# Optimization experiments

Measured on AMD Instinct MI355X. Metric: run time of the kernel, lower is better.

The kernel has to match this reference:

```python
import jax, jax.numpy as jnp
import numpy as np

S, N, C_M, C_Z, C, H = 256, 384, 64, 128, 32, 8


def _layer_norm(x, w, b, eps=1e-5):
    mu = x.mean(axis=-1, keepdims=True)
    var = x.var(axis=-1, keepdims=True)
    return (x - mu) / jnp.sqrt(var + eps) * w + b


def setup_inputs() -> dict:
    key = jax.random.key(0)
    ks = jax.random.split(key, 8)
    m = jax.random.normal(ks[0], (S, N, C_M), dtype=jnp.float32)
    z = jax.random.normal(ks[1], (N, N, C_Z), dtype=jnp.float32)
    single_mask = jax.random.bernoulli(ks[2], 0.9, (N,))
    scale = 0.02
    return {
        "m": m,
        "z": z,
        "single_mask": single_mask,
        "ln_m_w": jnp.ones((C_M,), jnp.float32),
        "ln_m_b": jnp.zeros((C_M,), jnp.float32),
        "ln_z_w": jnp.ones((C_Z,), jnp.float32),
        "ln_z_b": jnp.zeros((C_Z,), jnp.float32),
        "w_v": jax.random.normal(ks[3], (C_M, H * C), jnp.float32) * scale,
        "w_b": jax.random.normal(ks[4], (C_Z, H), jnp.float32) * scale,
        "w_g": jax.random.normal(ks[5], (C_M, H * C), jnp.float32) * scale,
        "w_out": jax.random.normal(ks[6], (H * C, C_M), jnp.float32) * scale,
    }


def reference(m, z, single_mask, ln_m_w, ln_m_b, ln_z_w, ln_z_b, w_v, w_b, w_g, w_out):
    # m: [s, i, c_m], z: [i, j, c_z], single_mask: [j] bool
    m_ln = _layer_norm(m, ln_m_w, ln_m_b)
    v = (m_ln @ w_v).reshape(S, N, H, C)          # [s, j, h, c]
    b = _layer_norm(z, ln_z_w, ln_z_b) @ w_b      # [i, j, h]
    g = jax.nn.sigmoid(m_ln @ w_g)                # [s, i, h*c]
    # mask broadcast over j axis: [..., None, :, None]
    b = b + jnp.where(single_mask[None, :, None], 0.0, -1e9)
    w = jax.nn.softmax(b, axis=-2)                # softmax over j
    o = jnp.einsum('ijh,sjhc->sihc', w, v)        # [s, i, h, c]
    o = g * o.reshape(S, N, H * C)
    return o @ w_out                               # [s, i, c_m]
```

## Files before the change

kernel.cpp:

```cpp
#include <hip/hip_runtime.h>
#include <math.h>


#define SS 256
#define NN 384
#define CM 64
#define CZ 128
#define HH 8
#define HC 256
#define NV 25165824

typedef __attribute__((ext_vector_type(8))) short short8v;
typedef __attribute__((ext_vector_type(8))) unsigned short ushort8v;
typedef __attribute__((ext_vector_type(4))) unsigned short ushort4v;
typedef __attribute__((ext_vector_type(4))) float f32x4;

static __device__ __forceinline__ float bf2f(unsigned short u) {
    union { unsigned int i; float f; } x; x.i = ((unsigned int)u) << 16; return x.f;
}
static __device__ __forceinline__ unsigned short f2bf(float f) {
    union { float f; unsigned int i; } x; x.f = f;
    unsigned int r = x.i + 0x7FFFu + ((x.i >> 16) & 1u);
    return (unsigned short)(r >> 16);
}
static __device__ __forceinline__ void gload_lds16(const void* g, void* l) {
    __builtin_amdgcn_global_load_lds((const __attribute__((address_space(1))) void*)g,
                                     (__attribute__((address_space(3))) void*)l, 16, 0, 0);
}

__global__ __launch_bounds__(384) void k0_mask(const unsigned int* __restrict__ mu,
                                               float* __restrict__ mterm)
{
    __shared__ int byteLayout;
    if (threadIdx.x == 0) byteLayout = 0;
    __syncthreads();
    if (threadIdx.x < 96) {
        unsigned int u = mu[threadIdx.x];
        if (u != 0u && u != 1u && u != 0x3F800000u) atomicOr(&byteLayout, 1);
    }
    __syncthreads();
    const int j = threadIdx.x;
    int val;
    if (byteLayout) val = ((const unsigned char*)mu)[j];
    else            val = (mu[j] != 0u);
    mterm[j] = val ? 0.0f : -1e9f;
}

__global__ __launch_bounds__(256) void k1a_stageB(
    const float* __restrict__ w_v, const float* __restrict__ w_g,
    unsigned short* __restrict__ BTg)
{
    const int col = blockIdx.x * 4 + (threadIdx.x >> 6);
    const int k   = threadIdx.x & 63;
    float w = (col < 256) ? w_v[k * 256 + col] : w_g[k * 256 + (col - 256)];
    BTg[col * 64 + (k ^ ((col & 7) << 3))] = f2bf(w);
}

__global__ __launch_bounds__(128) void k2a_stageW(
    const float* __restrict__ lnw, const float* __restrict__ lnb, const float* __restrict__ w_b,
    unsigned short* __restrict__ w2bf, float* __restrict__ consts)
{
    __shared__ float pA[128][8], pB[128][8];
    const int c = threadIdx.x;
    float lw = lnw[c], lb = lnb[c];
    float4 wb0 = *(const float4*)&w_b[c * 8];
    float4 wb1 = *(const float4*)&w_b[c * 8 + 4];
    float wv[8] = {wb0.x, wb0.y, wb0.z, wb0.w, wb1.x, wb1.y, wb1.z, wb1.w};
    #pragma unroll
    for (int h = 0; h < 8; h++) {
        w2bf[h * CZ + c]       = f2bf(lw * wv[h]);
        w2bf[(8 + h) * CZ + c] = 0;
        pA[c][h] = lw * wv[h];
        pB[c][h] = lb * wv[h];
    }
    __syncthreads();
    if (c < 8) {
        float A = 0.f, B = 0.f;
        for (int q = 0; q < 128; q++) { A += pA[q][c]; B += pB[q][c]; }
        consts[c] = A; consts[16 + c] = B;
        consts[8 + c] = 0.f; consts[24 + c] = 0.f;
    }
}

__global__ __launch_bounds__(256) void k1n_ln(
    const float* __restrict__ m, const float* __restrict__ lnw, const float* __restrict__ lnb,
    unsigned short* __restrict__ mln)
{
    const int tid = threadIdx.x, wid = tid >> 6, lane = tid & 63;
    const int rowBase = blockIdx.x * 64 + wid * 16;
    const float lw = lnw[lane], lb = lnb[lane];
    #pragma unroll 4
    for (int rr = 0; rr < 16; rr++) {
        int row = rowBase + rr;
        float x = m[(size_t)row * CM + lane];
        float s1 = x, s2 = x * x;
        #pragma unroll
        for (int off = 32; off; off >>= 1) {
            s1 += __shfl_xor(s1, off);
            s2 += __shfl_xor(s2, off);
        }
        float mu  = s1 * (1.0f / CM);
        float var = s2 * (1.0f / CM) - mu * mu;
        float y = (x - mu) * rsqrtf(var + 1e-5f) * lw + lb;
        mln[(size_t)row * CM + (lane ^ ((row & 7) << 3))] = f2bf(y);
    }
}

__global__ __launch_bounds__(256) void k1b_vg(
    const unsigned short* __restrict__ BTg, const unsigned short* __restrict__ mln,
    unsigned short* __restrict__ vT, unsigned short* __restrict__ gout)
{
    __shared__ unsigned short Wl[16384];
    __shared__ unsigned short Al[4096];
    const int tid = threadIdx.x, wid = tid >> 6, lane = tid & 63;
    const int rl = lane & 15, kc = lane >> 4;
    const int rowBase = blockIdx.x * 64;
    const int s = rowBase / NN, j0 = rowBase - s * NN;
    const int fam = blockIdx.y;

    #pragma unroll
    for (int it = 0; it < 8; it++) {
        int eoff = (wid * 8 + it) * 512;
        gload_lds16(BTg + fam * 16384 + eoff + lane * 8, (void*)((char*)Wl + eoff * 2));
    }
    #pragma unroll
    for (int it = 0; it < 2; it++) {
        int eoff = (wid * 2 + it) * 512;
        gload_lds16(mln + (size_t)rowBase * CM + eoff + lane * 8, (void*)((char*)Al + eoff * 2));
    }
    __syncthreads();

    f32x4 acc[4][4] = {};
    #pragma unroll
    for (int ks = 0; ks < 2; ks++) {
        short8v wf[4], al[4];
        #pragma unroll
        for (int q = 0; q < 4; q++) {
            int col = wid * 64 + q * 16 + rl;
            wf[q] = *(const short8v*)&Wl[(col * 64 + ks * 32 + kc * 8) ^ ((col & 7) << 3)];
            int row = q * 16 + rl;
            al[q] = *(const short8v*)&Al[(row * 64 + ks * 32 + kc * 8) ^ ((row & 7) << 3)];
        }
        if (fam == 0) {
            #pragma unroll
            for (int mi = 0; mi < 4; mi++)
                #pragma unroll
                for (int nf = 0; nf < 4; nf++)
                    acc[mi][nf] = __builtin_amdgcn_mfma_f32_16x16x32_bf16(al[mi], wf[nf], acc[mi][nf], 0, 0, 0);
        } else {
            #pragma unroll
            for (int mi = 0; mi < 4; mi++)
                #pragma unroll
                for (int nf = 0; nf < 4; nf++)
                    acc[mi][nf] = __builtin_amdgcn_mfma_f32_16x16x32_bf16(wf[mi], al[nf], acc[mi][nf], 0, 0, 0);
        }
    }

    if (fam == 0) {
        #pragma unroll
        for (int mi = 0; mi < 4; mi++) {
            const int jb = j0 + mi * 16 + kc * 4;
            #pragma unroll
            for (int nf = 0; nf < 4; nf++) {
                int hc = wid * 64 + nf * 16 + rl;
                size_t vrow = (size_t)((hc >> 5) * 8192 + s * 32 + (hc & 31));
                ushort4v o4;
                #pragma unroll
                for (int r = 0; r < 4; r++) o4[r] = f2bf(acc[mi][nf][r]);
                *(ushort4v*)&vT[vrow * NN + jb] = o4;
            }
        }
    } else {
        #pragma unroll
        for (int mi = 0; mi < 4; mi++) {
            const int hcb = wid * 64 + mi * 16 + kc * 4;
            #pragma unroll
            for (int nf = 0; nf < 4; nf++) {
                int row = rowBase + nf * 16 + rl;
                ushort4v o4;
                #pragma unroll
                for (int r = 0; r < 4; r++)
                    o4[r] = f2bf(1.0f / (1.0f + expf(-acc[mi][nf][r])));
                *(ushort4v*)&gout[(size_t)row * HC + hcb] = o4;
            }
        }
    }
}

__global__ __launch_bounds__(256) void k2_mfma(
    const float* __restrict__ z, const unsigned short* __restrict__ w2bf,
    const float* __restrict__ consts, const float* __restrict__ mterm,
    unsigned short* __restrict__ wbl)
{
    __shared__ float st[4][16][2];
    const int tid = threadIdx.x, wid = tid >> 6, lane = tid & 63;
    const int rl = lane & 15, kc = lane >> 4;
    const int rowBase = blockIdx.x * 64 + wid * 16;
    const int i = rowBase / NN, j0 = rowBase - i * NN;
    const float* zr = z + (size_t)(rowBase + rl) * CZ + kc * 8;

    float s1 = 0.f, s2 = 0.f;
    short8v af[4];
    #pragma unroll
    for (int ks = 0; ks < 4; ks++) {
        float4 z0 = *(const float4*)(zr + ks * 32);
        float4 z1 = *(const float4*)(zr + ks * 32 + 4);
        float zz[8] = {z0.x, z0.y, z0.z, z0.w, z1.x, z1.y, z1.z, z1.w};
        short8v a;
        #pragma unroll
        for (int q = 0; q < 8; q++) {
            s1 += zz[q];
            s2 += zz[q] * zz[q];
            a[q] = (short)f2bf(zz[q]);
        }
        af[ks] = a;
    }
    s1 += __shfl_xor(s1, 16); s2 += __shfl_xor(s2, 16);
    s1 += __shfl_xor(s1, 32); s2 += __shfl_xor(s2, 32);
    if (kc == 0) { st[wid][rl][0] = s1; st[wid][rl][1] = s2; }

    f32x4 acc = {};
    #pragma unroll
    for (int ks = 0; ks < 4; ks++) {
        short8v b = *(const short8v*)&w2bf[rl * CZ + ks * 32 + kc * 8];
        acc = __builtin_amdgcn_mfma_f32_16x16x32_bf16(af[ks], b, acc, 0, 0, 0);
    }
    __syncthreads();

    const float Ah = consts[rl], Bh = consts[16 + rl];
    unsigned short pv[4];
    #pragma unroll
    for (int reg = 0; reg < 4; reg++) {
        int r = 4 * kc + reg;
        float S1 = st[wid][r][0], S2 = st[wid][r][1];
        float mu   = S1 * (1.0f / CZ);
        float var  = S2 * (1.0f / CZ) - mu * mu;
        float rstd = rsqrtf(var + 1e-5f);
        float b = rstd * acc[reg] - rstd * mu * Ah + Bh + mterm[j0 + r];
        pv[reg] = f2bf(b);
    }
    if (rl < 8) {
        ushort4v o4 = {pv[0], pv[1], pv[2], pv[3]};
        *(ushort4v*)&wbl[((size_t)rl * NN + i) * NN + j0 + 4 * kc] = o4;
    }
}

__global__ __launch_bounds__(256) void k3_softmax(unsigned short* __restrict__ wbl)
{
    const int tid = threadIdx.x, wave = tid >> 6, lane = tid & 63;
    const int row = blockIdx.x * 4 + wave;
    unsigned short* p = wbl + (size_t)row * NN;
    float x[6];
    float mx = -1e30f;
    #pragma unroll
    for (int e = 0; e < 6; e++) { x[e] = bf2f(p[lane + e * 64]); mx = fmaxf(mx, x[e]); }
    #pragma unroll
    for (int off = 32; off; off >>= 1) mx = fmaxf(mx, __shfl_xor(mx, off));
    float sum = 0.f;
    #pragma unroll
    for (int e = 0; e < 6; e++) { x[e] = expf(x[e] - mx); sum += x[e]; }
    #pragma unroll
    for (int off = 32; off; off >>= 1) sum += __shfl_xor(sum, off);
    float inv = 1.0f / sum;
    #pragma unroll
    for (int e = 0; e < 6; e++) p[lane + e * 64] = f2bf(x[e] * inv);
}

__global__ __launch_bounds__(256) void k4_mfma(
    const unsigned short* __restrict__ wbf, const unsigned short* __restrict__ vT,
    unsigned short* __restrict__ ob)
{
    __shared__ unsigned short Al[128 * 32];
    __shared__ unsigned short Bl[128 * 32];
    const int tid  = threadIdx.x;
    const int wid  = tid >> 6, lane = tid & 63;
    const int wm   = wid >> 1, wn = wid & 1;
    const int h    = blockIdx.z;
    const int i0   = blockIdx.y * 128;
    const int n0   = blockIdx.x * 128;
    const unsigned short* Ag = wbf + (size_t)h * NN * NN;
    const unsigned short* Bg = vT  + (size_t)h * 8192 * NN;

    f32x4 acc[4][4] = {};

    const int lrow = lane >> 2, lchunk = lane & 3;
    for (int k0 = 0; k0 < NN; k0 += 32) {
        #pragma unroll
        for (int q = 0; q < 2; q++) {
            int issue = wid * 2 + q;
            int r = issue * 16 + lrow;
            gload_lds16(Ag + (size_t)(i0 + r) * NN + k0 + lchunk * 8,
                        (void*)((char*)Al + issue * 1024));
            gload_lds16(Bg + (size_t)(n0 + r) * NN + k0 + lchunk * 8,
                        (void*)((char*)Bl + issue * 1024));
        }
        __syncthreads();

        short8v a[4], b[4];
        #pragma unroll
        for (int mi = 0; mi < 4; mi++)
            a[mi] = *(const short8v*)&Al[(wm * 64 + mi * 16 + (lane & 15)) * 32 + (lane >> 4) * 8];
        #pragma unroll
        for (int ni = 0; ni < 4; ni++)
            b[ni] = *(const short8v*)&Bl[(wn * 64 + ni * 16 + (lane & 15)) * 32 + (lane >> 4) * 8];
        #pragma unroll
        for (int mi = 0; mi < 4; mi++)
            #pragma unroll
            for (int ni = 0; ni < 4; ni++)
                acc[mi][ni] = __builtin_amdgcn_mfma_f32_16x16x32_bf16(a[mi], b[ni], acc[mi][ni], 0, 0, 0);
        __syncthreads();
    }

    #pragma unroll
    for (int mi = 0; mi < 4; mi++) {
        const int ibase = i0 + wm * 64 + mi * 16 + ((lane >> 4) << 2);
        #pragma unroll
        for (int ni = 0; ni < 4; ni++) {
            const int n = n0 + wn * 64 + ni * 16 + (lane & 15);
            const int s = n >> 5, c = n & 31;
            #pragma unroll
            for (int r = 0; r < 4; r++)
                ob[((size_t)s * NN + (ibase + r)) * HC + (h << 5) + c] = f2bf(acc[mi][ni][r]);
        }
    }
}

__global__ __launch_bounds__(256) void k5_mfma(
    const unsigned short* __restrict__ ob, const unsigned short* __restrict__ g,
    const float* __restrict__ w_out, float* __restrict__ out)
{
    __shared__ unsigned short WT[64 * 256];
    const int tid = threadIdx.x, wid = tid >> 6, lane = tid & 63;
    #pragma unroll
    for (int e = 0; e < 16; e++) {
        int fidx = (tid + e * 256) * 4;
        float4 w4 = *(const float4*)&w_out[fidx];
        int k = fidx >> 6, c0 = fidx & 63;
        float wv[4] = {w4.x, w4.y, w4.z, w4.w};
        #pragma unroll
        for (int q = 0; q < 4; q++) {
            int c = c0 + q;
            WT[(((c << 8) + k)) ^ ((c & 7) << 3)] = f2bf(wv[q]);
        }
    }
    __syncthreads();

    const size_t rowbase = (size_t)blockIdx.x * 64 + wid * 16;
    const int arow = lane & 15, achunk = lane >> 4;
    const unsigned short* op = ob + (rowbase + arow) * HC + achunk * 8;
    const unsigned short* gp = g  + (rowbase + arow) * HC + achunk * 8;

    f32x4 acc[4] = {};
    #pragma unroll
    for (int ks = 0; ks < 8; ks++) {
        ushort8v o8 = *(const ushort8v*)(op + ks * 32);
        ushort8v g8 = *(const ushort8v*)(gp + ks * 32);
        short8v a;
        #pragma unroll
        for (int q = 0; q < 8; q++)
            a[q] = (short)f2bf(bf2f(o8[q]) * bf2f(g8[q]));
        #pragma unroll
        for (int nf = 0; nf < 4; nf++) {
            const int c = nf * 16 + arow;
            short8v b = *(const short8v*)&WT[(((c << 8) + ks * 32 + achunk * 8)) ^ ((c & 7) << 3)];
            acc[nf] = __builtin_amdgcn_mfma_f32_16x16x32_bf16(a, b, acc[nf], 0, 0, 0);
        }
    }
    #pragma unroll
    for (int nf = 0; nf < 4; nf++)
        #pragma unroll
        for (int r = 0; r < 4; r++)
            out[(rowbase + achunk * 4 + r) * CM + nf * 16 + arow] = acc[nf][r];
}

extern "C" void kernel_launch(void* const* d_in, const int* in_sizes, int n_in,
                              void* d_out, int out_size, void* d_ws, size_t ws_size,
                              hipStream_t stream)
{
    const float* m      = (const float*)d_in[0];
    const float* z      = (const float*)d_in[1];
    const unsigned int* mask_raw = (const unsigned int*)d_in[2];
    const float* ln_m_w = (const float*)d_in[3];
    const float* ln_m_b = (const float*)d_in[4];
    const float* ln_z_w = (const float*)d_in[5];
    const float* ln_z_b = (const float*)d_in[6];
    const float* w_v    = (const float*)d_in[7];
    const float* w_b    = (const float*)d_in[8];
    const float* w_g    = (const float*)d_in[9];
    const float* w_out  = (const float*)d_in[10];
    float* out = (float*)d_out;

    float* mterm = (float*)d_ws;
    unsigned short* wbl = (unsigned short*)(mterm + 384);
    unsigned short* vT  = wbl + 1179648;
    unsigned short* g   = vT + NV;
    unsigned short* ob  = g + NV;
    unsigned short* BTg = ob + NV;
    unsigned short* w2bf = BTg + 32768;
    float* consts = (float*)(w2bf + 2048);
    unsigned short* mln = ob;

    k0_mask<<<1, 384, 0, stream>>>(mask_raw, mterm);
    k1a_stageB<<<128, 256, 0, stream>>>(w_v, w_g, BTg);
    k2a_stageW<<<1, 128, 0, stream>>>(ln_z_w, ln_z_b, w_b, w2bf, consts);
    k1n_ln<<<1536, 256, 0, stream>>>(m, ln_m_w, ln_m_b, mln);
    k1b_vg<<<dim3(1536, 2), 256, 0, stream>>>(BTg, mln, vT, g);
    k2_mfma<<<2304, 256, 0, stream>>>(z, w2bf, consts, mterm, wbl);
    k3_softmax<<<768, 256, 0, stream>>>(wbl);
    k4_mfma<<<dim3(64, 3, 8), 256, 0, stream>>>(wbl, vT, ob);
    k5_mfma<<<1536, 256, 0, stream>>>(ob, g, w_out, out);
}
```

Baseline: 146.4 us.

## Drop LDS staging in v/g projection and process two row tiles per block

The v/g projection kernel no longer stages weights and activations through shared memory. Each wave now loads its weight fragments straight from global memory into registers once, then reuses them across two 64-row tiles, so the grid is halved. This removes the LDS round trip and the barrier, and halves redundant weight loads per row. The cost is more register pressure and uncoalesced direct global fragment loads that depend on the pre-swizzled layout.

```diff
diff --git a/kernel.cpp b/kernel.cpp
--- a/kernel.cpp
+++ b/kernel.cpp
@@ -110,78 +110,80 @@
     const unsigned short* __restrict__ BTg, const unsigned short* __restrict__ mln,
     unsigned short* __restrict__ vT, unsigned short* __restrict__ gout)
 {
-    __shared__ unsigned short Wl[16384];
-    __shared__ unsigned short Al[4096];
     const int tid = threadIdx.x, wid = tid >> 6, lane = tid & 63;
     const int rl = lane & 15, kc = lane >> 4;
-    const int rowBase = blockIdx.x * 64;
-    const int s = rowBase / NN, j0 = rowBase - s * NN;
     const int fam = blockIdx.y;
 
-    #pragma unroll
-    for (int it = 0; it < 8; it++) {
-        int eoff = (wid * 8 + it) * 512;
-        gload_lds16(BTg + fam * 16384 + eoff + lane * 8, (void*)((char*)Wl + eoff * 2));
-    }
-    #pragma unroll
-    for (int it = 0; it < 2; it++) {
-        int eoff = (wid * 2 + it) * 512;
-        gload_lds16(mln + (size_t)rowBase * CM + eoff + lane * 8, (void*)((char*)Al + eoff * 2));
-    }
-    __syncthreads();
-
-    f32x4 acc[4][4] = {};
-    #pragma unroll
-    for (int ks = 0; ks < 2; ks++) {
-        short8v wf[4], al[4];
+    short8v wf[2][4];
+    #pragma unroll
+    for (int ks = 0; ks < 2; ks++)
         #pragma unroll
         for (int q = 0; q < 4; q++) {
             int col = wid * 64 + q * 16 + rl;
-            wf[q] = *(const short8v*)&Wl[(col * 64 + ks * 32 + kc * 8) ^ ((col & 7) << 3)];
-            int row = q * 16 + rl;
-            al[q] = *(const short8v*)&Al[(row * 64 + ks * 32 + kc * 8) ^ ((row & 7) << 3)];
-        }
+            wf[ks][q] = *(const short8v*)&BTg[fam * 16384 + col * 64 +
+                                             ((ks * 32 + kc * 8) ^ ((col & 7) << 3))];
+        }
+
+    #pragma unroll
+    for (int t = 0; t < 2; t++) {
+        const int rowBase = blockIdx.x * 128 + t * 64;
+        const int s = rowBase / NN, j0 = rowBase - s * NN;
+
+        short8v al[2][4];
+        #pragma unroll
+        for (int ks = 0; ks < 2; ks++)
+            #pragma unroll
+            for (int q = 0; q < 4; q++) {
+                int row = rowBase + q * 16 + rl;
+                al[ks][q] = *(const short8v*)&mln[(size_t)row * CM +
+                                                  ((ks * 32 + kc * 8) ^ ((rl & 7) << 3))];
+            }
+
+        f32x4 acc[4][4] = {};
+        #pragma unroll
+        for (int ks = 0; ks < 2; ks++) {
+            if (fam == 0) {
+                #pragma unroll
+                for (int mi = 0; mi < 4; mi++)
+                    #pragma unroll
+                    for (int nf = 0; nf < 4; nf++)
+                        acc[mi][nf] = __builtin_amdgcn_mfma_f32_16x16x32_bf16(al[ks][mi], wf[ks][nf], acc[mi][nf], 0, 0, 0);
+            } else {
+                #pragma unroll
+                for (int mi = 0; mi < 4; mi++)
+                    #pragma unroll
+                    for (int nf = 0; nf < 4; nf++)
+                        acc[mi][nf] = __builtin_amdgcn_mfma_f32_16x16x32_bf16(wf[ks][mi], al[ks][nf], acc[mi][nf], 0, 0, 0);
+            }
+        }
+
         if (fam == 0) {
             #pragma unroll
-            for (int mi = 0; mi < 4; mi++)
+            for (int mi = 0; mi < 4; mi++) {
+                const int jb = j0 + mi * 16 + kc * 4;
                 #pragma unroll
-                for (int nf = 0; nf < 4; nf++)
-                    acc[mi][nf] = __builtin_amdgcn_mfma_f32_16x16x32_bf16(al[mi], wf[nf], acc[mi][nf], 0, 0, 0);
+                for (int nf = 0; nf < 4; nf++) {
+                    int hc = wid * 64 + nf * 16 + rl;
+                    size_t vrow = (size_t)((hc >> 5) * 8192 + s * 32 + (hc & 31));
+                    ushort4v o4;
+                    #pragma unroll
+                    for (int r = 0; r < 4; r++) o4[r] = f2bf(acc[mi][nf][r]);
+                    *(ushort4v*)&vT[vrow * NN + jb] = o4;
+                }
+            }
         } else {
             #pragma unroll
-            for (int mi = 0; mi < 4; mi++)
+            for (int mi = 0; mi < 4; mi++) {
+                const int hcb = wid * 64 + mi * 16 + kc * 4;
                 #pragma unroll
-                for (int nf = 0; nf < 4; nf++)
-                    acc[mi][nf] = __builtin_amdgcn_mfma_f32_16x16x32_bf16(wf[mi], al[nf], acc[mi][nf], 0, 0, 0);
-        }
-    }
-
-    if (fam == 0) {
-        #pragma unroll
-        for (int mi = 0; mi < 4; mi++) {
-            const int jb = j0 + mi * 16 + kc * 4;
-            #pragma unroll
-            for (int nf = 0; nf < 4; nf++) {
-                int hc = wid * 64 + nf * 16 + rl;
-                size_t vrow = (size_t)((hc >> 5) * 8192 + s * 32 + (hc & 31));
-                ushort4v o4;
-                #pragma unroll
-                for (int r = 0; r < 4; r++) o4[r] = f2bf(acc[mi][nf][r]);
-                *(ushort4v*)&vT[vrow * NN + jb] = o4;
-            }
-        }
-    } else {
-        #pragma unroll
-        for (int mi = 0; mi < 4; mi++) {
-            const int hcb = wid * 64 + mi * 16 + kc * 4;
-            #pragma unroll
-            for (int nf = 0; nf < 4; nf++) {
-                int row = rowBase + nf * 16 + rl;
-                ushort4v o4;
-                #pragma unroll
-                for (int r = 0; r < 4; r++)
-                    o4[r] = f2bf(1.0f / (1.0f + expf(-acc[mi][nf][r])));
-                *(ushort4v*)&gout[(size_t)row * HC + hcb] = o4;
+                for (int nf = 0; nf < 4; nf++) {
+                    int row = rowBase + nf * 16 + rl;
+                    ushort4v o4;
+                    #pragma unroll
+                    for (int r = 0; r < 4; r++)
+                        o4[r] = f2bf(1.0f / (1.0f + expf(-acc[mi][nf][r])));
+                    *(ushort4v*)&gout[(size_t)row * HC + hcb] = o4;
+                }
             }
         }
     }
@@ -404,7 +406,7 @@
     k1a_stageB<<<128, 256, 0, stream>>>(w_v, w_g, BTg);
     k2a_stageW<<<1, 128, 0, stream>>>(ln_z_w, ln_z_b, w_b, w2bf, consts);
     k1n_ln<<<1536, 256, 0, stream>>>(m, ln_m_w, ln_m_b, mln);
-    k1b_vg<<<dim3(1536, 2), 256, 0, stream>>>(BTg, mln, vT, g);
+    k1b_vg<<<dim3(768, 2), 256, 0, stream>>>(BTg, mln, vT, g);
     k2_mfma<<<2304, 256, 0, stream>>>(z, w2bf, consts, mterm, wbl);
     k3_softmax<<<768, 256, 0, stream>>>(wbl);
     k4_mfma<<<dim3(64, 3, 8), 256, 0, stream>>>(wbl, vT, ob);
```

New measurement: 149.2 us. About the same (+2.0%).
